# Kernel tuning notes

Measured on AMD Instinct MI355X. Metric: run time of the kernel, lower is better.

The kernel has to match this reference:

```python
import jax, jax.numpy as jnp
import numpy as np

N, B, L, E = 64, 128, 4096, 16
BN_EPS = 1e-5


def setup_inputs() -> dict:
    key = jax.random.key(0)
    ks = jax.random.split(key, 6)
    feat = jax.random.normal(ks[0], (N, B, L), dtype=jnp.float32)
    # Glorot-ish scaled linear weights
    Wl = jax.random.normal(ks[1], (L, E), dtype=jnp.float32) * (1.0 / np.sqrt(L))
    Wr = jax.random.normal(ks[2], (L, E), dtype=jnp.float32) * (1.0 / np.sqrt(L))
    Wm = jax.random.normal(ks[3], (L, L), dtype=jnp.float32) * (1.0 / np.sqrt(L))
    return {
        "feat": feat,
        "Wl": Wl, "bl": jnp.zeros((E,), jnp.float32),
        "Wr": Wr, "br": jnp.zeros((E,), jnp.float32),
        "Wm": Wm, "bm": jnp.zeros((L,), jnp.float32),
        "gamma": jnp.ones((N * N,), jnp.float32),
        "beta": jnp.zeros((N * N,), jnp.float32),
        "bias": jnp.zeros((L,), jnp.float32),
    }


def reference(feat, Wl, bl, Wr, br, Wm, bm, gamma, beta, bias):
    # feat: (N, B, L) node time series
    # Attention projections (lookup_l / lookup_r): Linear(L -> E)
    att_l = feat @ Wl + bl                      # (N, B, E) on src nodes
    att_r = feat @ Wr + br                      # (N, B, E) on dst nodes

    # Feature extractor: MLP Linear(L, L) + ReLU over the time axis
    out = jax.nn.relu(jnp.einsum('nbl,kl->nbk', feat, Wm) + bm)   # (N, B, L)

    # Edge scores on the complete graph: e[d, s, b] = att_l[src=s] . att_r[dst=d]
    e = jnp.einsum('sbe,dbe->dsb', att_l, att_r)                  # (Nd, Ns, B)

    # BatchNorm1d over N*N edge channels (training-mode batch statistics)
    ef = e.reshape(N * N, B)
    mu = ef.mean(axis=1, keepdims=True)
    var = ef.var(axis=1, keepdims=True)
    ef = gamma[:, None] * (ef - mu) * jax.lax.rsqrt(var + BN_EPS) + beta[:, None]
    e = ef.reshape(N, N, B)

    # edge_softmax: normalize over incoming edges (src axis) per destination node
    w = jax.nn.softmax(e, axis=1)                                  # (Nd, Ns, B)

    # Weighted neighbor aggregation + bias
    rst = jnp.einsum('dsb,sbl->dbl', w, out) + bias                # (N, B, L)
    return rst
```

## Files before the change

### kernel.cpp

```cpp
#include <hip/hip_runtime.h>
#include <stdint.h>
#include <stddef.h>

#define NN 64
#define BB 128
#define LL 4096
#define EE 16

typedef __attribute__((ext_vector_type(4))) float f32x4;
typedef __attribute__((ext_vector_type(2))) float f32x2;
typedef __attribute__((ext_vector_type(8))) short short8;
typedef __attribute__((ext_vector_type(4))) unsigned short u16x4;

__device__ __forceinline__ unsigned short f2bf(float f) {
  union { float f; unsigned u; } v; v.f = f;
  unsigned r = v.u + 0x7FFFu + ((v.u >> 16) & 1u);
  return (unsigned short)(r >> 16);
}
__device__ __forceinline__ float bf2f(unsigned short h) {
  union { unsigned u; float f; } v; v.u = ((unsigned)h) << 16;
  return v.f;
}
__device__ __forceinline__ void gload16(const void* g, void* l) {
  __builtin_amdgcn_global_load_lds((const __attribute__((address_space(1))) void*)g,
                                   (__attribute__((address_space(3))) void*)l,
                                   16, 0, 0);
}

#define MFMA(a, b, c) __builtin_amdgcn_mfma_f32_16x16x32_bf16((a), (b), (c), 0, 0, 0)

__global__ __launch_bounds__(256) void k_cvtw(const float* __restrict__ Wm,
    const float* __restrict__ Wl, const float* __restrict__ Wr,
    unsigned short* __restrict__ wm_bf, unsigned short* __restrict__ wt_bf) {
  int bid = blockIdx.x;
  if (bid < 2048) {
    int i = bid * 256 + threadIdx.x;
    for (; i < (LL * LL / 4); i += 2048 * 256) {
      f32x4 v = ((const f32x4*)Wm)[i];
      u16x4 o;
      o[0] = f2bf(v[0]); o[1] = f2bf(v[1]); o[2] = f2bf(v[2]); o[3] = f2bf(v[3]);
      ((u16x4*)wm_bf)[i] = o;
    }
  } else {
    int u = (bid - 2048) * 256 + threadIdx.x;
    int e = u >> 6;
    int kb = (u & 63) * 64;
    const float* src = (e < 16) ? (Wl + e) : (Wr + (e - 16));
    for (int k = kb; k < kb + 64; ++k)
      wt_bf[(size_t)e * LL + k] = f2bf(src[(size_t)k * 16]);
  }
}

__global__ __launch_bounds__(256) void k_attF(const float* __restrict__ feat,
    const unsigned short* __restrict__ wt_bf,
    unsigned short* __restrict__ feat_bf, float* __restrict__ attP) {
  __shared__ __align__(16) unsigned short alds[64 * 512];
  const int t = threadIdx.x, lane = t & 63, w = t >> 6;
  const int rowBase = blockIdx.x * 64;
  const int kBase = blockIdx.y * 2048;
  const int rr = lane & 15, gg8 = (lane >> 4) * 8;
  f32x4 acc0 = {}, acc1 = {};
  const unsigned short* b0P = wt_bf + (size_t)rr * LL;
  const unsigned short* b1P = wt_bf + (size_t)(16 + rr) * LL;
  for (int c = 0; c < 4; ++c) {
    const int k0 = kBase + c * 512;
    __syncthreads();
    #pragma unroll
    for (int u = 0; u < 32; ++u) {
      int unit = t + u * 256;
      int row = unit >> 7, col4 = unit & 127;
      size_t gi = (size_t)(rowBase + row) * LL + k0 + col4 * 4;
      f32x4 v = *(const f32x4*)&feat[gi];
      u16x4 o; o[0] = f2bf(v[0]); o[1] = f2bf(v[1]); o[2] = f2bf(v[2]); o[3] = f2bf(v[3]);
      *(u16x4*)&feat_bf[gi] = o;
      int byte = (row * 1024 + col4 * 8) ^ ((row & 7) << 4);
      *(u16x4*)((char*)alds + byte) = o;
    }
    __syncthreads();
    const int arow = w * 16 + rr;
    const char* aBase = (const char*)alds + arow * 1024;
    const int axor = (arow & 7) << 4;
    #pragma unroll 4
    for (int ks = 0; ks < 16; ++ks) {
      int abyte = ((ks * 32 + gg8) * 2) ^ axor;
      short8 av = *(const short8*)(aBase + abyte);
      short8 b0 = *(const short8*)(b0P + k0 + ks * 32 + gg8);
      short8 b1 = *(const short8*)(b1P + k0 + ks * 32 + gg8);
      acc0 = MFMA(av, b0, acc0);
      acc1 = MFMA(av, b1, acc1);
    }
  }
  const int orow = rowBase + w * 16 + (lane >> 4) * 4;
  float* P = attP + (size_t)blockIdx.y * (8192 * 32);
  #pragma unroll
  for (int j = 0; j < 4; ++j) {
    P[(size_t)(orow + j) * 32 + rr]      = acc0[j];
    P[(size_t)(orow + j) * 32 + 16 + rr] = acc1[j];
  }
}

__global__ __launch_bounds__(256) void k_edge(const float* __restrict__ attP,
    const float* __restrict__ bl, const float* __restrict__ br,
    const float* __restrict__ gamma, const float* __restrict__ beta,
    float* __restrict__ w_t) {
  __shared__ __align__(16) float attr[BB][20];
  __shared__ float el[NN][BB + 1];
  __shared__ float part[NN][4][2];
  __shared__ float sc[NN], sh[NN];
  int d = blockIdx.x, t = threadIdx.x;
  for (int i = t; i < 2048; i += 256) {
    int b = i >> 4, e = i & 15;
    float v2 = br[e];
    #pragma unroll
    for (int c = 0; c < 2; ++c)
      v2 += attP[(size_t)c * (8192 * 32) + ((size_t)d * 128 + b) * 32 + 16 + e];
    attr[b][e] = v2;
  }
  float blv[16];
  #pragma unroll
  for (int e = 0; e < 16; ++e) blv[e] = bl[e];
  __syncthreads();
  for (int v = t; v < NN * BB; v += 256) {
    int s = v >> 7, b = v & 127;
    float al[16];
    #pragma unroll
    for (int e = 0; e < 16; ++e) al[e] = blv[e];
    #pragma unroll
    for (int c = 0; c < 2; ++c) {
      const f32x4* p = (const f32x4*)&attP[(size_t)c * (8192 * 32) + ((size_t)s * 128 + b) * 32];
      #pragma unroll
      for (int q = 0; q < 4; ++q) {
        f32x4 x = p[q];
        al[q * 4 + 0] += x[0]; al[q * 4 + 1] += x[1];
        al[q * 4 + 2] += x[2]; al[q * 4 + 3] += x[3];
      }
    }
    float acc = 0.f;
    #pragma unroll
    for (int e = 0; e < 16; ++e) acc += al[e] * attr[b][e];
    el[s][b] = acc;
  }
  __syncthreads();
  {
    int s = t >> 2, q = t & 3;
    float sum = 0.f, ss = 0.f;
    for (int b = q * 32; b < q * 32 + 32; ++b) { float x = el[s][b]; sum += x; ss += x * x; }
    part[s][q][0] = sum; part[s][q][1] = ss;
  }
  __syncthreads();
  if (t < 64) {
    float sum = 0.f, ss = 0.f;
    #pragma unroll
    for (int q = 0; q < 4; ++q) { sum += part[t][q][0]; ss += part[t][q][1]; }
    float mu = sum * (1.f / 128.f);
    float var = ss * (1.f / 128.f) - mu * mu;
    int c = d * 64 + t;
    float a = gamma[c] * rsqrtf(fmaxf(var, 0.f) + 1e-5f);
    sc[t] = a; sh[t] = beta[c] - mu * a;
  }
  __syncthreads();
  if (t < 128) {
    int b = t;
    float y[64];
    float m = -1e30f;
    #pragma unroll
    for (int s = 0; s < 64; ++s) { y[s] = sc[s] * el[s][b] + sh[s]; m = fmaxf(m, y[s]); }
    float sum = 0.f;
    #pragma unroll
    for (int s = 0; s < 64; ++s) { y[s] = __expf(y[s] - m); sum += y[s]; }
    float inv = 1.f / sum;
    float* wp = &w_t[((size_t)b * 64 + d) * 64];
    #pragma unroll
    for (int s4 = 0; s4 < 16; ++s4) {
      f32x4 o;
      o[0] = y[s4 * 4 + 0] * inv; o[1] = y[s4 * 4 + 1] * inv;
      o[2] = y[s4 * 4 + 2] * inv; o[3] = y[s4 * 4 + 3] * inv;
      *(f32x4*)&wp[s4 * 4] = o;
    }
  }
}

#define LDS_A 0
#define LDS_B 65536
#define BAR   __builtin_amdgcn_s_barrier()
#define VM8   asm volatile("s_waitcnt vmcnt(8)" ::: "memory")
#define VM4   asm volatile("s_waitcnt vmcnt(4)" ::: "memory")
#define VM2   asm volatile("s_waitcnt vmcnt(2)" ::: "memory")
#define VM0   asm volatile("s_waitcnt vmcnt(0)" ::: "memory")
#define PRIO1 __builtin_amdgcn_s_setprio(1)
#define PRIO0 __builtin_amdgcn_s_setprio(0)
#define STAGE2(g0, g1, ldsoff) do { \
    gload16((g0), lds_raw + (ldsoff) + tid16); \
    gload16((g1), lds_raw + (ldsoff) + 8192 + tid16); } while (0)

__global__ __launch_bounds__(512, 2) void k_gemm8(const unsigned short* __restrict__ A,
    const unsigned short* __restrict__ Bm, const float* __restrict__ bm,
    unsigned short* __restrict__ C) {
  __shared__ __align__(16) char lds_raw[131072];
  const int tid = threadIdx.x;
  const int lane = tid & 63, wave = tid >> 6;
  const int wm = wave >> 2, wn = wave & 3;
  int bid = blockIdx.x;
  int swz = (bid & 7) * 64 + (bid >> 3);
  int tM = swz >> 4, tN = swz & 15;
  const size_t rowBase = (size_t)tM * 256, colBase = (size_t)tN * 256;
  const int tid16 = tid * 16;
  const int o0 = tid16, o1 = tid16 + 8192;
  const int r0s = (o0 & 1023) >> 6, r1s = (o1 & 1023) >> 6;
  const int row0 = (o0 >> 10) * 16 + r0s, row1 = (o1 >> 10) * 16 + r1s;
  const int col0 = (((o0 >> 4) & 3) ^ ((r0s >> 3) << 1)) * 8;
  const int col1 = (((o1 >> 4) & 3) ^ ((r1s >> 3) << 1)) * 8;
  const unsigned short* aR0 = A  + (rowBase + row0) * LL + col0;
  const unsigned short* aR1 = A  + (rowBase + row1) * LL + col1;
  const unsigned short* bR0 = Bm + (colBase + row0) * LL + col0;
  const unsigned short* bR1 = Bm + (colBase + row1) * LL + col1;
  const int rr = lane & 15, gg = lane >> 4;
  const int rdswz = rr * 64 + ((gg ^ ((rr >> 3) << 1)) << 4);
  f32x4 acc[8][4] = {};
  STAGE2(aR0 +  0, aR1 +  0, LDS_A + 0);
  STAGE2(bR0 +  0, bR1 +  0, LDS_B + 0);
  STAGE2(aR0 + 32, aR1 + 32, LDS_A + 16384);
  STAGE2(bR0 + 32, bR1 + 32, LDS_B + 16384);
  STAGE2(bR0 + 64, bR1 + 64, LDS_B + 32768);
  STAGE2(aR0 + 64, aR1 + 64, LDS_A + 32768);
  VM8;
  BAR;
  #pragma unroll 2
  for (int t = 0; t < 64; ++t) {
    const int d = t & 1;
    const char* pA = lds_raw + LDS_A + d * 32768 + wm * 8192 + rdswz;
    const char* pB = lds_raw + LDS_B + d * 32768 + wn * 4096 + rdswz;
    short8 ar[4], bf4[4];
    #pragma unroll
    for (int i = 0; i < 4; ++i) bf4[i] = *(const short8*)(pB + i * 1024);
    #pragma unroll
    for (int i = 0; i < 4; ++i) ar[i] = *(const short8*)(pA + i * 1024);
    if (t <= 62) { size_t kk = (size_t)(t + 1) * 64 + 32;
      STAGE2(aR0 + kk, aR1 + kk, LDS_A + ((t + 1) & 1) * 32768 + 16384); }
    BAR; PRIO1;
    #pragma unroll
    for (int i = 0; i < 4; ++i) {
      acc[i][0] = MFMA(ar[i], bf4[0], acc[i][0]);
      acc[i][1] = MFMA(ar[i], bf4[1], acc[i][1]);
      acc[i][2] = MFMA(ar[i], bf4[2], acc[i][2]);
      acc[i][3] = MFMA(ar[i], bf4[3], acc[i][3]);
    }
    PRIO0; BAR;
    #pragma unroll
    for (int i = 0; i < 4; ++i) ar[i] = *(const short8*)(pA + 4096 + i * 1024);
    if (t <= 61) { size_t kk = (size_t)(t + 2) * 64;
      STAGE2(bR0 + kk, bR1 + kk, LDS_B + d * 32768); }
    BAR; PRIO1;
    #pragma unroll
    for (int i = 0; i < 4; ++i) {
      acc[4 + i][0] = MFMA(ar[i], bf4[0], acc[4 + i][0]);
      acc[4 + i][1] = MFMA(ar[i], bf4[1], acc[4 + i][1]);
      acc[4 + i][2] = MFMA(ar[i], bf4[2], acc[4 + i][2]);
      acc[4 + i][3] = MFMA(ar[i], bf4[3], acc[4 + i][3]);
    }
    PRIO0;
    if (t <= 61) { VM4; } else if (t == 62) { VM2; } else { VM0; }
    BAR;
    #pragma unroll
    for (int i = 0; i < 4; ++i) bf4[i] = *(const short8*)(pB + 16384 + i * 1024);
    #pragma unroll
    for (int i = 0; i < 4; ++i) ar[i] = *(const short8*)(pA + 16384 + i * 1024);
    if (t <= 61) { size_t kk = (size_t)(t + 2) * 64;
      STAGE2(aR0 + kk, aR1 + kk, LDS_A + d * 32768); }
    BAR; PRIO1;
    #pragma unroll
    for (int i = 0; i < 4; ++i) {
      acc[i][0] = MFMA(ar[i], bf4[0], acc[i][0]);
      acc[i][1] = MFMA(ar[i], bf4[1], acc[i][1]);
      acc[i][2] = MFMA(ar[i], bf4[2], acc[i][2]);
      acc[i][3] = MFMA(ar[i], bf4[3], acc[i][3]);
    }
    PRIO0; BAR;
    #pragma unroll
    for (int i = 0; i < 4; ++i) ar[i] = *(const short8*)(pA + 16384 + 4096 + i * 1024);
    if (t <= 62) { size_t kk = (size_t)(t + 1) * 64 + 32;
      STAGE2(bR0 + kk, bR1 + kk, LDS_B + ((t + 1) & 1) * 32768 + 16384); }
    BAR; PRIO1;
    #pragma unroll
    for (int i = 0; i < 4; ++i) {
      acc[4 + i][0] = MFMA(ar[i], bf4[0], acc[4 + i][0]);
      acc[4 + i][1] = MFMA(ar[i], bf4[1], acc[4 + i][1]);
      acc[4 + i][2] = MFMA(ar[i], bf4[2], acc[4 + i][2]);
      acc[4 + i][3] = MFMA(ar[i], bf4[3], acc[4 + i][3]);
    }
    PRIO0;
    if (t <= 61) { VM8; } else { VM4; }
    BAR;
  }
  VM0;
  const int co = lane & 15, ro4 = (lane >> 4) * 4;
  #pragma unroll
  for (int mig = 0; mig < 8; ++mig) {
    size_t r0 = rowBase + (size_t)wm * 128 + mig * 16 + ro4;
    #pragma unroll
    for (int nj = 0; nj < 4; ++nj) {
      size_t c = colBase + (size_t)wn * 64 + nj * 16 + co;
      float bc = bm[c];
      #pragma unroll
      for (int j = 0; j < 4; ++j) {
        float v = acc[mig][nj][j] + bc;
        v = fmaxf(v, 0.f);
        C[(r0 + j) * LL + c] = f2bf(v);
      }
    }
  }
}

__global__ __launch_bounds__(256) void k_agg2(const float* __restrict__ w_t,
    const unsigned short* __restrict__ outb, const float* __restrict__ bias,
    float* __restrict__ rst) {
  int b = blockIdx.y;
  int t = threadIdx.x;
  int l0 = blockIdx.x * 512 + t * 2;
  float oA[64], oB[64];
  #pragma unroll
  for (int s = 0; s < 64; ++s) {
    unsigned u = *(const unsigned*)&outb[((size_t)s * BB + b) * LL + l0];
    oA[s] = bf2f((unsigned short)(u & 0xFFFF));
    oB[s] = bf2f((unsigned short)(u >> 16));
  }
  const float* wb = w_t + (size_t)b * 4096;
  float bs0 = bias[l0], bs1 = bias[l0 + 1];
  #pragma unroll 2
  for (int d = 0; d < 64; ++d) {
    const float* wr = wb + d * 64;
    float a0 = 0.f, a1 = 0.f;
    #pragma unroll
    for (int q = 0; q < 16; ++q) {
      f32x4 wq = *(const f32x4*)&wr[q * 4];
      #pragma unroll
      for (int j = 0; j < 4; ++j) {
        float wv = wq[j];
        a0 += wv * oA[q * 4 + j];
        a1 += wv * oB[q * 4 + j];
      }
    }
    f32x2 o; o[0] = a0 + bs0; o[1] = a1 + bs1;
    *(f32x2*)&rst[((size_t)d * BB + b) * LL + l0] = o;
  }
}

extern "C" void kernel_launch(void* const* d_in, const int* in_sizes, int n_in,
                              void* d_out, int out_size, void* d_ws, size_t ws_size,
                              hipStream_t stream) {
  (void)in_sizes; (void)n_in; (void)out_size; (void)ws_size;
  const float* feat  = (const float*)d_in[0];
  const float* Wl    = (const float*)d_in[1];
  const float* bl    = (const float*)d_in[2];
  const float* Wr    = (const float*)d_in[3];
  const float* br    = (const float*)d_in[4];
  const float* Wm    = (const float*)d_in[5];
  const float* bm    = (const float*)d_in[6];
  const float* gamma = (const float*)d_in[7];
  const float* beta  = (const float*)d_in[8];
  const float* bias  = (const float*)d_in[9];
  char* ws = (char*)d_ws;
  unsigned short* feat_bf = (unsigned short*)(ws);
  unsigned short* wm_bf   = (unsigned short*)(ws + 67108864ull);
  unsigned short* out_bf  = (unsigned short*)(ws + 100663296ull);
  float* attP  = (float*)(ws + 167772160ull);
  float* w_t   = (float*)(ws + 169869312ull);
  unsigned short* wt_bf = (unsigned short*)(ws + 171966464ull);
  float* rst = (float*)d_out;

  k_cvtw<<<dim3(2056), dim3(256), 0, stream>>>(Wm, Wl, Wr, wm_bf, wt_bf);
  k_attF<<<dim3(128, 2), dim3(256), 0, stream>>>(feat, wt_bf, feat_bf, attP);
  k_edge<<<dim3(64), dim3(256), 0, stream>>>(attP, bl, br, gamma, beta, w_t);
  k_gemm8<<<dim3(512), dim3(512), 0, stream>>>(feat_bf, wm_bf, bm, out_bf);
  k_agg2<<<dim3(8, 128), dim3(256), 0, stream>>>(w_t, out_bf, bias, rst);
}
```

Before: 442.3 us.

## Register double-buffer LDS fragments in GEMM main loop to overlap reads with MFMA

```diff
diff --git a/kernel.cpp b/kernel.cpp
--- a/kernel.cpp
+++ b/kernel.cpp
@@ -184,8 +184,8 @@
 #define LDS_B 65536
 #define BAR   __builtin_amdgcn_s_barrier()
 #define VM8   asm volatile("s_waitcnt vmcnt(8)" ::: "memory")
+#define VM6   asm volatile("s_waitcnt vmcnt(6)" ::: "memory")
 #define VM4   asm volatile("s_waitcnt vmcnt(4)" ::: "memory")
-#define VM2   asm volatile("s_waitcnt vmcnt(2)" ::: "memory")
 #define VM0   asm volatile("s_waitcnt vmcnt(0)" ::: "memory")
 #define PRIO1 __builtin_amdgcn_s_setprio(1)
 #define PRIO0 __builtin_amdgcn_s_setprio(0)
@@ -217,80 +217,92 @@
   const int rr = lane & 15, gg = lane >> 4;
   const int rdswz = rr * 64 + ((gg ^ ((rr >> 3) << 1)) << 4);
   f32x4 acc[8][4] = {};
+  short8 aA[4], aB[4], bA[4], bB[4];
   STAGE2(aR0 +  0, aR1 +  0, LDS_A + 0);
   STAGE2(bR0 +  0, bR1 +  0, LDS_B + 0);
   STAGE2(aR0 + 32, aR1 + 32, LDS_A + 16384);
   STAGE2(bR0 + 32, bR1 + 32, LDS_B + 16384);
+  STAGE2(aR0 + 64, aR1 + 64, LDS_A + 32768);
   STAGE2(bR0 + 64, bR1 + 64, LDS_B + 32768);
-  STAGE2(aR0 + 64, aR1 + 64, LDS_A + 32768);
   VM8;
   BAR;
+  {
+    const char* pA0 = lds_raw + LDS_A + wm * 8192 + rdswz;
+    const char* pB0 = lds_raw + LDS_B + wn * 4096 + rdswz;
+    #pragma unroll
+    for (int i = 0; i < 4; ++i) aA[i] = *(const short8*)(pA0 + i * 1024);
+    #pragma unroll
+    for (int j = 0; j < 4; ++j) bA[j] = *(const short8*)(pB0 + j * 1024);
+  }
   #pragma unroll 2
   for (int t = 0; t < 64; ++t) {
     const int d = t & 1;
-    const char* pA = lds_raw + LDS_A + d * 32768 + wm * 8192 + rdswz;
-    const char* pB = lds_raw + LDS_B + d * 32768 + wn * 4096 + rdswz;
-    short8 ar[4], bf4[4];
-    #pragma unroll
-    for (int i = 0; i < 4; ++i) bf4[i] = *(const short8*)(pB + i * 1024);
-    #pragma unroll
-    for (int i = 0; i < 4; ++i) ar[i] = *(const short8*)(pA + i * 1024);
+    const char* pA  = lds_raw + LDS_A + d * 32768 + wm * 8192 + rdswz;
+    const char* pB  = lds_raw + LDS_B + d * 32768 + wn * 4096 + rdswz;
+    const char* pA2 = lds_raw + LDS_A + (d ^ 1) * 32768 + wm * 8192 + rdswz;
+    const char* pB2 = lds_raw + LDS_B + (d ^ 1) * 32768 + wn * 4096 + rdswz;
+    #pragma unroll
+    for (int i = 0; i < 4; ++i) aB[i] = *(const short8*)(pA + 4096 + i * 1024);
     if (t <= 62) { size_t kk = (size_t)(t + 1) * 64 + 32;
       STAGE2(aR0 + kk, aR1 + kk, LDS_A + ((t + 1) & 1) * 32768 + 16384); }
-    BAR; PRIO1;
+    PRIO1;
     #pragma unroll
     for (int i = 0; i < 4; ++i) {
-      acc[i][0] = MFMA(ar[i], bf4[0], acc[i][0]);
-      acc[i][1] = MFMA(ar[i], bf4[1], acc[i][1]);
-      acc[i][2] = MFMA(ar[i], bf4[2], acc[i][2]);
-      acc[i][3] = MFMA(ar[i], bf4[3], acc[i][3]);
+      acc[i][0] = MFMA(aA[i], bA[0], acc[i][0]);
+      acc[i][1] = MFMA(aA[i], bA[1], acc[i][1]);
+      acc[i][2] = MFMA(aA[i], bA[2], acc[i][2]);
+      acc[i][3] = MFMA(aA[i], bA[3], acc[i][3]);
+    }
+    PRIO0;
+    if (t <= 62) { VM6; } else { VM0; }
+    BAR;
+    #pragma unroll
+    for (int i = 0; i < 4; ++i) aA[i] = *(const short8*)(pA + 16384 + i * 1024);
+    #pragma unroll
+    for (int j = 0; j < 4; ++j) bB[j] = *(const short8*)(pB + 16384 + j * 1024);
+    if (t <= 62) { size_t kk = (size_t)(t + 1) * 64 + 32;
+      STAGE2(bR0 + kk, bR1 + kk, LDS_B + ((t + 1) & 1) * 32768 + 16384); }
+    PRIO1;
+    #pragma unroll
+    for (int i = 0; i < 4; ++i) {
+      acc[4 + i][0] = MFMA(aB[i], bA[0], acc[4 + i][0]);
+      acc[4 + i][1] = MFMA(aB[i], bA[1], acc[4 + i][1]);
+      acc[4 + i][2] = MFMA(aB[i], bA[2], acc[4 + i][2]);
+      acc[4 + i][3] = MFMA(aB[i], bA[3], acc[4 + i][3]);
     }
     PRIO0; BAR;
     #pragma unroll
-    for (int i = 0; i < 4; ++i) ar[i] = *(const short8*)(pA + 4096 + i * 1024);
+    for (int i = 0; i < 4; ++i) aB[i] = *(const short8*)(pA + 16384 + 4096 + i * 1024);
+    if (t <= 61) { size_t kk = (size_t)(t + 2) * 64;
+      STAGE2(aR0 + kk, aR1 + kk, LDS_A + d * 32768); }
+    PRIO1;
+    #pragma unroll
+    for (int i = 0; i < 4; ++i) {
+      acc[i][0] = MFMA(aA[i], bB[0], acc[i][0]);
+      acc[i][1] = MFMA(aA[i], bB[1], acc[i][1]);
+      acc[i][2] = MFMA(aA[i], bB[2], acc[i][2]);
+      acc[i][3] = MFMA(aA[i], bB[3], acc[i][3]);
+    }
+    PRIO0;
+    if (t <= 61) { VM6; } else if (t == 62) { VM4; } else { VM0; }
+    BAR;
+    if (t < 63) {
+      #pragma unroll
+      for (int i = 0; i < 4; ++i) aA[i] = *(const short8*)(pA2 + i * 1024);
+      #pragma unroll
+      for (int j = 0; j < 4; ++j) bA[j] = *(const short8*)(pB2 + j * 1024);
+    }
     if (t <= 61) { size_t kk = (size_t)(t + 2) * 64;
       STAGE2(bR0 + kk, bR1 + kk, LDS_B + d * 32768); }
-    BAR; PRIO1;
+    PRIO1;
     #pragma unroll
     for (int i = 0; i < 4; ++i) {
-      acc[4 + i][0] = MFMA(ar[i], bf4[0], acc[4 + i][0]);
-      acc[4 + i][1] = MFMA(ar[i], bf4[1], acc[4 + i][1]);
-      acc[4 + i][2] = MFMA(ar[i], bf4[2], acc[4 + i][2]);
-      acc[4 + i][3] = MFMA(ar[i], bf4[3], acc[4 + i][3]);
-    }
-    PRIO0;
-    if (t <= 61) { VM4; } else if (t == 62) { VM2; } else { VM0; }
-    BAR;
-    #pragma unroll
-    for (int i = 0; i < 4; ++i) bf4[i] = *(const short8*)(pB + 16384 + i * 1024);
-    #pragma unroll
-    for (int i = 0; i < 4; ++i) ar[i] = *(const short8*)(pA + 16384 + i * 1024);
-    if (t <= 61) { size_t kk = (size_t)(t + 2) * 64;
-      STAGE2(aR0 + kk, aR1 + kk, LDS_A + d * 32768); }
-    BAR; PRIO1;
-    #pragma unroll
-    for (int i = 0; i < 4; ++i) {
-      acc[i][0] = MFMA(ar[i], bf4[0], acc[i][0]);
-      acc[i][1] = MFMA(ar[i], bf4[1], acc[i][1]);
-      acc[i][2] = MFMA(ar[i], bf4[2], acc[i][2]);
-      acc[i][3] = MFMA(ar[i], bf4[3], acc[i][3]);
+      acc[4 + i][0] = MFMA(aB[i], bB[0], acc[4 + i][0]);
+      acc[4 + i][1] = MFMA(aB[i], bB[1], acc[4 + i][1]);
+      acc[4 + i][2] = MFMA(aB[i], bB[2], acc[4 + i][2]);
+      acc[4 + i][3] = MFMA(aB[i], bB[3], acc[4 + i][3]);
     }
     PRIO0; BAR;
-    #pragma unroll
-    for (int i = 0; i < 4; ++i) ar[i] = *(const short8*)(pA + 16384 + 4096 + i * 1024);
-    if (t <= 62) { size_t kk = (size_t)(t + 1) * 64 + 32;
-      STAGE2(bR0 + kk, bR1 + kk, LDS_B + ((t + 1) & 1) * 32768 + 16384); }
-    BAR; PRIO1;
-    #pragma unroll
-    for (int i = 0; i < 4; ++i) {
-      acc[4 + i][0] = MFMA(ar[i], bf4[0], acc[4 + i][0]);
-      acc[4 + i][1] = MFMA(ar[i], bf4[1], acc[4 + i][1]);
-      acc[4 + i][2] = MFMA(ar[i], bf4[2], acc[4 + i][2]);
-      acc[4 + i][3] = MFMA(ar[i], bf4[3], acc[4 + i][3]);
-    }
-    PRIO0;
-    if (t <= 61) { VM8; } else { VM4; }
-    BAR;
   }
   VM0;
   const int co = lane & 15, ro4 = (lane >> 4) * 4;
```

Result: slower. 751.2 us (+69.8%).

## Replace 256x256 GEMM with 128x256 tile, 3-stage LDS pipeline, 4 waves

Applied to the files above, without the earlier changes.

```diff
diff --git a/kernel.cpp b/kernel.cpp
--- a/kernel.cpp
+++ b/kernel.cpp
@@ -180,126 +180,73 @@
   }
 }
 
-#define LDS_A 0
-#define LDS_B 65536
 #define BAR   __builtin_amdgcn_s_barrier()
-#define VM8   asm volatile("s_waitcnt vmcnt(8)" ::: "memory")
-#define VM4   asm volatile("s_waitcnt vmcnt(4)" ::: "memory")
-#define VM2   asm volatile("s_waitcnt vmcnt(2)" ::: "memory")
+#define VM6   asm volatile("s_waitcnt vmcnt(6)" ::: "memory")
 #define VM0   asm volatile("s_waitcnt vmcnt(0)" ::: "memory")
+#define NOVM  do {} while (0)
 #define PRIO1 __builtin_amdgcn_s_setprio(1)
 #define PRIO0 __builtin_amdgcn_s_setprio(0)
-#define STAGE2(g0, g1, ldsoff) do { \
-    gload16((g0), lds_raw + (ldsoff) + tid16); \
-    gload16((g1), lds_raw + (ldsoff) + 8192 + tid16); } while (0)
-
-__global__ __launch_bounds__(512, 2) void k_gemm8(const unsigned short* __restrict__ A,
+
+#define STAGE6(STG, KK) do { \
+    gload16(aG0 + (KK),            ldsm + (STG) * 8192 + tid16); \
+    gload16(aG0 + 64 * LL + (KK),  ldsm + (STG) * 8192 + 4096 + tid16); \
+    gload16(bG0 + (KK),            ldsm + 24576 + (STG) * 16384 + tid16); \
+    gload16(bG0 + 64 * LL + (KK),  ldsm + 24576 + (STG) * 16384 + 4096 + tid16); \
+    gload16(bG0 + 128 * LL + (KK), ldsm + 24576 + (STG) * 16384 + 8192 + tid16); \
+    gload16(bG0 + 192 * LL + (KK), ldsm + 24576 + (STG) * 16384 + 12288 + tid16); \
+  } while (0)
+
+#define GITER(T, CUR, STG, DOSTAGE, VMW) do { \
+    const char* pA = ldsm + (CUR) * 8192 + wm * 4096 + rdswz; \
+    const char* pB = ldsm + 24576 + (CUR) * 16384 + wn * 8192 + rdswz; \
+    short8 af[4], bf[8]; \
+    _Pragma("unroll") for (int mi = 0; mi < 4; ++mi) af[mi] = *(const short8*)(pA + mi * 1024); \
+    _Pragma("unroll") for (int nj = 0; nj < 8; ++nj) bf[nj] = *(const short8*)(pB + nj * 1024); \
+    if (DOSTAGE) { STAGE6(STG, (size_t)((T) + 2) * 32); } \
+    PRIO1; \
+    _Pragma("unroll") for (int mi = 0; mi < 4; ++mi) \
+      _Pragma("unroll") for (int nj = 0; nj < 8; ++nj) \
+        acc[mi][nj] = MFMA(af[mi], bf[nj], acc[mi][nj]); \
+    PRIO0; VMW; BAR; \
+  } while (0)
+
+__global__ __launch_bounds__(256, 2) void k_gemmW(const unsigned short* __restrict__ A,
     const unsigned short* __restrict__ Bm, const float* __restrict__ bm,
     unsigned short* __restrict__ C) {
-  __shared__ __align__(16) char lds_raw[131072];
+  __shared__ __align__(16) char ldsm[73728];
   const int tid = threadIdx.x;
   const int lane = tid & 63, wave = tid >> 6;
-  const int wm = wave >> 2, wn = wave & 3;
+  const int wm = wave >> 1, wn = wave & 1;
   int bid = blockIdx.x;
-  int swz = (bid & 7) * 64 + (bid >> 3);
+  int swz = (bid & 7) * 128 + (bid >> 3);
   int tM = swz >> 4, tN = swz & 15;
-  const size_t rowBase = (size_t)tM * 256, colBase = (size_t)tN * 256;
+  const size_t rowBase = (size_t)tM * 128, colBase = (size_t)tN * 256;
   const int tid16 = tid * 16;
-  const int o0 = tid16, o1 = tid16 + 8192;
-  const int r0s = (o0 & 1023) >> 6, r1s = (o1 & 1023) >> 6;
-  const int row0 = (o0 >> 10) * 16 + r0s, row1 = (o1 >> 10) * 16 + r1s;
-  const int col0 = (((o0 >> 4) & 3) ^ ((r0s >> 3) << 1)) * 8;
-  const int col1 = (((o1 >> 4) & 3) ^ ((r1s >> 3) << 1)) * 8;
-  const unsigned short* aR0 = A  + (rowBase + row0) * LL + col0;
-  const unsigned short* aR1 = A  + (rowBase + row1) * LL + col1;
-  const unsigned short* bR0 = Bm + (colBase + row0) * LL + col0;
-  const unsigned short* bR1 = Bm + (colBase + row1) * LL + col1;
+  const int srow = tid >> 2;
+  const int qx = (tid & 3) ^ (((tid >> 5) & 1) << 1);
+  const unsigned short* aG0 = A  + (rowBase + srow) * LL + qx * 8;
+  const unsigned short* bG0 = Bm + (colBase + srow) * LL + qx * 8;
   const int rr = lane & 15, gg = lane >> 4;
   const int rdswz = rr * 64 + ((gg ^ ((rr >> 3) << 1)) << 4);
-  f32x4 acc[8][4] = {};
-  STAGE2(aR0 +  0, aR1 +  0, LDS_A + 0);
-  STAGE2(bR0 +  0, bR1 +  0, LDS_B + 0);
-  STAGE2(aR0 + 32, aR1 + 32, LDS_A + 16384);
-  STAGE2(bR0 + 32, bR1 + 32, LDS_B + 16384);
-  STAGE2(bR0 + 64, bR1 + 64, LDS_B + 32768);
-  STAGE2(aR0 + 64, aR1 + 64, LDS_A + 32768);
-  VM8;
+  f32x4 acc[4][8] = {};
+  STAGE6(0, 0);
+  STAGE6(1, 32);
+  VM6;
   BAR;
-  #pragma unroll 2
-  for (int t = 0; t < 64; ++t) {
-    const int d = t & 1;
-    const char* pA = lds_raw + LDS_A + d * 32768 + wm * 8192 + rdswz;
-    const char* pB = lds_raw + LDS_B + d * 32768 + wn * 4096 + rdswz;
-    short8 ar[4], bf4[4];
-    #pragma unroll
-    for (int i = 0; i < 4; ++i) bf4[i] = *(const short8*)(pB + i * 1024);
-    #pragma unroll
-    for (int i = 0; i < 4; ++i) ar[i] = *(const short8*)(pA + i * 1024);
-    if (t <= 62) { size_t kk = (size_t)(t + 1) * 64 + 32;
-      STAGE2(aR0 + kk, aR1 + kk, LDS_A + ((t + 1) & 1) * 32768 + 16384); }
-    BAR; PRIO1;
-    #pragma unroll
-    for (int i = 0; i < 4; ++i) {
-      acc[i][0] = MFMA(ar[i], bf4[0], acc[i][0]);
-      acc[i][1] = MFMA(ar[i], bf4[1], acc[i][1]);
-      acc[i][2] = MFMA(ar[i], bf4[2], acc[i][2]);
-      acc[i][3] = MFMA(ar[i], bf4[3], acc[i][3]);
-    }
-    PRIO0; BAR;
-    #pragma unroll
-    for (int i = 0; i < 4; ++i) ar[i] = *(const short8*)(pA + 4096 + i * 1024);
-    if (t <= 61) { size_t kk = (size_t)(t + 2) * 64;
-      STAGE2(bR0 + kk, bR1 + kk, LDS_B + d * 32768); }
-    BAR; PRIO1;
-    #pragma unroll
-    for (int i = 0; i < 4; ++i) {
-      acc[4 + i][0] = MFMA(ar[i], bf4[0], acc[4 + i][0]);
-      acc[4 + i][1] = MFMA(ar[i], bf4[1], acc[4 + i][1]);
-      acc[4 + i][2] = MFMA(ar[i], bf4[2], acc[4 + i][2]);
-      acc[4 + i][3] = MFMA(ar[i], bf4[3], acc[4 + i][3]);
-    }
-    PRIO0;
-    if (t <= 61) { VM4; } else if (t == 62) { VM2; } else { VM0; }
-    BAR;
-    #pragma unroll
-    for (int i = 0; i < 4; ++i) bf4[i] = *(const short8*)(pB + 16384 + i * 1024);
-    #pragma unroll
-    for (int i = 0; i < 4; ++i) ar[i] = *(const short8*)(pA + 16384 + i * 1024);
-    if (t <= 61) { size_t kk = (size_t)(t + 2) * 64;
-      STAGE2(aR0 + kk, aR1 + kk, LDS_A + d * 32768); }
-    BAR; PRIO1;
-    #pragma unroll
-    for (int i = 0; i < 4; ++i) {
-      acc[i][0] = MFMA(ar[i], bf4[0], acc[i][0]);
-      acc[i][1] = MFMA(ar[i], bf4[1], acc[i][1]);
-      acc[i][2] = MFMA(ar[i], bf4[2], acc[i][2]);
-      acc[i][3] = MFMA(ar[i], bf4[3], acc[i][3]);
-    }
-    PRIO0; BAR;
-    #pragma unroll
-    for (int i = 0; i < 4; ++i) ar[i] = *(const short8*)(pA + 16384 + 4096 + i * 1024);
-    if (t <= 62) { size_t kk = (size_t)(t + 1) * 64 + 32;
-      STAGE2(bR0 + kk, bR1 + kk, LDS_B + ((t + 1) & 1) * 32768 + 16384); }
-    BAR; PRIO1;
-    #pragma unroll
-    for (int i = 0; i < 4; ++i) {
-      acc[4 + i][0] = MFMA(ar[i], bf4[0], acc[4 + i][0]);
-      acc[4 + i][1] = MFMA(ar[i], bf4[1], acc[4 + i][1]);
-      acc[4 + i][2] = MFMA(ar[i], bf4[2], acc[4 + i][2]);
-      acc[4 + i][3] = MFMA(ar[i], bf4[3], acc[4 + i][3]);
-    }
-    PRIO0;
-    if (t <= 61) { VM8; } else { VM4; }
-    BAR;
-  }
-  VM0;
+  for (int tb = 0; tb < 126; tb += 3) {
+    GITER(tb,     0, 2, 1, VM6);
+    GITER(tb + 1, 1, 0, 1, VM6);
+    GITER(tb + 2, 2, 1, 1, VM6);
+  }
+  GITER(126, 0, 0, 0, VM0);
+  GITER(127, 1, 0, 0, NOVM);
   const int co = lane & 15, ro4 = (lane >> 4) * 4;
   #pragma unroll
-  for (int mig = 0; mig < 8; ++mig) {
-    size_t r0 = rowBase + (size_t)wm * 128 + mig * 16 + ro4;
-    #pragma unroll
-    for (int nj = 0; nj < 4; ++nj) {
-      size_t c = colBase + (size_t)wn * 64 + nj * 16 + co;
+  for (int mig = 0; mig < 4; ++mig) {
+    size_t r0 = rowBase + (size_t)wm * 64 + mig * 16 + ro4;
+    #pragma unroll
+    for (int nj = 0; nj < 8; ++nj) {
+      size_t c = colBase + (size_t)wn * 128 + nj * 16 + co;
       float bc = bm[c];
       #pragma unroll
       for (int j = 0; j < 4; ++j) {
@@ -371,6 +318,6 @@
   k_cvtw<<<dim3(2056), dim3(256), 0, stream>>>(Wm, Wl, Wr, wm_bf, wt_bf);
   k_attF<<<dim3(128, 2), dim3(256), 0, stream>>>(feat, wt_bf, feat_bf, attP);
   k_edge<<<dim3(64), dim3(256), 0, stream>>>(attP, bl, br, gamma, beta, w_t);
-  k_gemm8<<<dim3(512), dim3(512), 0, stream>>>(feat_bf, wm_bf, bm, out_bf);
+  k_gemmW<<<dim3(1024), dim3(256), 0, stream>>>(feat_bf, wm_bf, bm, out_bf);
   k_agg2<<<dim3(8, 128), dim3(256), 0, stream>>>(w_t, out_bf, bias, rst);
 }
```

After: 466.2 us. 5.4% more time.

## Move feat bf16 conversion into weight-convert kernel and widen attention split-K

Applied to the files above, without the earlier changes.

```diff
diff --git a/kernel.cpp b/kernel.cpp
--- a/kernel.cpp
+++ b/kernel.cpp
@@ -29,20 +29,30 @@
 
 #define MFMA(a, b, c) __builtin_amdgcn_mfma_f32_16x16x32_bf16((a), (b), (c), 0, 0, 0)
 
-__global__ __launch_bounds__(256) void k_cvtw(const float* __restrict__ Wm,
+__global__ __launch_bounds__(256) void k_cvtAll(const float* __restrict__ Wm,
     const float* __restrict__ Wl, const float* __restrict__ Wr,
-    unsigned short* __restrict__ wm_bf, unsigned short* __restrict__ wt_bf) {
-  int bid = blockIdx.x;
+    const float* __restrict__ feat,
+    unsigned short* __restrict__ wm_bf, unsigned short* __restrict__ wt_bf,
+    unsigned short* __restrict__ feat_bf) {
+  int bid = blockIdx.x, t = threadIdx.x;
   if (bid < 2048) {
-    int i = bid * 256 + threadIdx.x;
-    for (; i < (LL * LL / 4); i += 2048 * 256) {
+    int i = bid * 256 + t;
+    const int n4 = LL * LL / 4;
+    for (; i < n4; i += 2048 * 256) {
       f32x4 v = ((const f32x4*)Wm)[i];
-      u16x4 o;
-      o[0] = f2bf(v[0]); o[1] = f2bf(v[1]); o[2] = f2bf(v[2]); o[3] = f2bf(v[3]);
+      u16x4 o; o[0] = f2bf(v[0]); o[1] = f2bf(v[1]); o[2] = f2bf(v[2]); o[3] = f2bf(v[3]);
       ((u16x4*)wm_bf)[i] = o;
     }
+  } else if (bid < 4096) {
+    int i = (bid - 2048) * 256 + t;
+    const int n4 = NN * BB * LL / 4;
+    for (; i < n4; i += 2048 * 256) {
+      f32x4 v = ((const f32x4*)feat)[i];
+      u16x4 o; o[0] = f2bf(v[0]); o[1] = f2bf(v[1]); o[2] = f2bf(v[2]); o[3] = f2bf(v[3]);
+      ((u16x4*)feat_bf)[i] = o;
+    }
   } else {
-    int u = (bid - 2048) * 256 + threadIdx.x;
+    int u = (bid - 4096) * 256 + t;
     int e = u >> 6;
     int kb = (u & 63) * 64;
     const float* src = (e < 16) ? (Wl + e) : (Wr + (e - 16));
@@ -51,39 +61,35 @@
   }
 }
 
-__global__ __launch_bounds__(256) void k_attF(const float* __restrict__ feat,
-    const unsigned short* __restrict__ wt_bf,
-    unsigned short* __restrict__ feat_bf, float* __restrict__ attP) {
-  __shared__ __align__(16) unsigned short alds[64 * 512];
+__global__ __launch_bounds__(256) void k_attM(const unsigned short* __restrict__ feat_bf,
+    const unsigned short* __restrict__ wt_bf, float* __restrict__ attP) {
+  __shared__ __align__(16) char alds[65536];
   const int t = threadIdx.x, lane = t & 63, w = t >> 6;
   const int rowBase = blockIdx.x * 64;
-  const int kBase = blockIdx.y * 2048;
-  const int rr = lane & 15, gg8 = (lane >> 4) * 8;
+  const int kBase = blockIdx.y * 1024;
+  const int rr = lane & 15, gg = lane >> 4, gg8 = gg * 8;
   f32x4 acc0 = {}, acc1 = {};
   const unsigned short* b0P = wt_bf + (size_t)rr * LL;
   const unsigned short* b1P = wt_bf + (size_t)(16 + rr) * LL;
-  for (int c = 0; c < 4; ++c) {
-    const int k0 = kBase + c * 512;
+  const int arow = w * 16 + rr;
+  const char* aBase = alds + arow * 1024;
+  const int axor = (arow & 7) << 4;
+  for (int ch = 0; ch < 2; ++ch) {
+    const int k0 = kBase + ch * 512;
     __syncthreads();
     #pragma unroll
-    for (int u = 0; u < 32; ++u) {
-      int unit = t + u * 256;
-      int row = unit >> 7, col4 = unit & 127;
-      size_t gi = (size_t)(rowBase + row) * LL + k0 + col4 * 4;
-      f32x4 v = *(const f32x4*)&feat[gi];
-      u16x4 o; o[0] = f2bf(v[0]); o[1] = f2bf(v[1]); o[2] = f2bf(v[2]); o[3] = f2bf(v[3]);
-      *(u16x4*)&feat_bf[gi] = o;
-      int byte = (row * 1024 + col4 * 8) ^ ((row & 7) << 4);
-      *(u16x4*)((char*)alds + byte) = o;
-    }
+    for (int p = 0; p < 16; ++p) {
+      int row = p * 4 + (t >> 6);
+      int colsw = ((t & 63) * 16) ^ ((row & 7) << 4);
+      const char* src = (const char*)feat_bf + (size_t)(rowBase + row) * (LL * 2)
+                        + (size_t)k0 * 2 + colsw;
+      gload16(src, alds + p * 4096 + t * 16);
+    }
+    asm volatile("s_waitcnt vmcnt(0)" ::: "memory");
     __syncthreads();
-    const int arow = w * 16 + rr;
-    const char* aBase = (const char*)alds + arow * 1024;
-    const int axor = (arow & 7) << 4;
     #pragma unroll 4
     for (int ks = 0; ks < 16; ++ks) {
-      int abyte = ((ks * 32 + gg8) * 2) ^ axor;
-      short8 av = *(const short8*)(aBase + abyte);
+      short8 av = *(const short8*)(aBase + ((ks * 64 + gg * 16) ^ axor));
       short8 b0 = *(const short8*)(b0P + k0 + ks * 32 + gg8);
       short8 b1 = *(const short8*)(b1P + k0 + ks * 32 + gg8);
       acc0 = MFMA(av, b0, acc0);
@@ -112,7 +118,7 @@
     int b = i >> 4, e = i & 15;
     float v2 = br[e];
     #pragma unroll
-    for (int c = 0; c < 2; ++c)
+    for (int c = 0; c < 4; ++c)
       v2 += attP[(size_t)c * (8192 * 32) + ((size_t)d * 128 + b) * 32 + 16 + e];
     attr[b][e] = v2;
   }
@@ -126,7 +132,7 @@
     #pragma unroll
     for (int e = 0; e < 16; ++e) al[e] = blv[e];
     #pragma unroll
-    for (int c = 0; c < 2; ++c) {
+    for (int c = 0; c < 4; ++c) {
       const f32x4* p = (const f32x4*)&attP[(size_t)c * (8192 * 32) + ((size_t)s * 128 + b) * 32];
       #pragma unroll
       for (int q = 0; q < 4; ++q) {
@@ -180,8 +186,6 @@
   }
 }
 
-#define LDS_A 0
-#define LDS_B 65536
 #define BAR   __builtin_amdgcn_s_barrier()
 #define VM8   asm volatile("s_waitcnt vmcnt(8)" ::: "memory")
 #define VM4   asm volatile("s_waitcnt vmcnt(4)" ::: "memory")
@@ -192,6 +196,8 @@
 #define STAGE2(g0, g1, ldsoff) do { \
     gload16((g0), lds_raw + (ldsoff) + tid16); \
     gload16((g1), lds_raw + (ldsoff) + 8192 + tid16); } while (0)
+#define LDS_A 0
+#define LDS_B 65536
 
 __global__ __launch_bounds__(512, 2) void k_gemm8(const unsigned short* __restrict__ A,
     const unsigned short* __restrict__ Bm, const float* __restrict__ bm,
@@ -364,12 +370,12 @@
   unsigned short* wm_bf   = (unsigned short*)(ws + 67108864ull);
   unsigned short* out_bf  = (unsigned short*)(ws + 100663296ull);
   float* attP  = (float*)(ws + 167772160ull);
-  float* w_t   = (float*)(ws + 169869312ull);
-  unsigned short* wt_bf = (unsigned short*)(ws + 171966464ull);
+  float* w_t   = (float*)(ws + 171966464ull);
+  unsigned short* wt_bf = (unsigned short*)(ws + 174063616ull);
   float* rst = (float*)d_out;
 
-  k_cvtw<<<dim3(2056), dim3(256), 0, stream>>>(Wm, Wl, Wr, wm_bf, wt_bf);
-  k_attF<<<dim3(128, 2), dim3(256), 0, stream>>>(feat, wt_bf, feat_bf, attP);
+  k_cvtAll<<<dim3(4104), dim3(256), 0, stream>>>(Wm, Wl, Wr, feat, wm_bf, wt_bf, feat_bf);
+  k_attM<<<dim3(128, 4), dim3(256), 0, stream>>>(feat_bf, wt_bf, attP);
   k_edge<<<dim3(64), dim3(256), 0, stream>>>(attP, bl, br, gamma, beta, w_t);
   k_gemm8<<<dim3(512), dim3(512), 0, stream>>>(feat_bf, wm_bf, bm, out_bf);
   k_agg2<<<dim3(8, 128), dim3(256), 0, stream>>>(w_t, out_bf, bias, rst);
```

After: 484.6 us. +9.6%, slower.
